# Optimization experiments

Hardware: AMD Instinct MI355X
Metric: run time of the kernel (lower is better)

Reference implementation:

```python
import jax, jax.numpy as jnp
import numpy as np

EPS_LN = 1e-5  # eqx.nn.LayerNorm default eps
DT_EPS = 1e-4  # softplus(dt) + 0.0001 in the module

H = 256  # hidden size
S = 256  # state size
B = 32
T = 4096


def setup_inputs() -> dict:
    key = jax.random.key(0)
    ks = jax.random.split(key, 8)
    sc = 1.0 / np.sqrt(H)
    return {
        "x": jax.random.normal(ks[0], (B, T, H), jnp.float32),
        "state0": jnp.zeros((B, S), jnp.float32),
        "in_to_state": jax.random.normal(ks[1], (S, H), jnp.float32) * sc,
        "state_to_hidden": jax.random.normal(ks[2], (H, S), jnp.float32) * sc,
        "direct": jax.random.normal(ks[3], (H,), jnp.float32) * sc,
        "a_diag": jax.random.normal(ks[4], (S,), jnp.float32),
        "g_diag": jax.random.normal(ks[5], (S,), jnp.float32),
        "dt": jax.random.normal(ks[6], (S,), jnp.float32) * 0.5 - 2.0,  # small timesteps
        "norm_w": jnp.ones((H,), jnp.float32),
        "norm_b": jnp.zeros((H,), jnp.float32),
        "out_w": jax.random.normal(ks[7], (H, H), jnp.float32) * sc,
        "out_b": jnp.zeros((H,), jnp.float32),
    }


def reference(x, state0, in_to_state, state_to_hidden, direct, a_diag, g_diag,
              dt, norm_w, norm_b, out_w, out_b):
    # Discretized diagonal oscillator coefficients (input-independent)
    dt_s = jax.nn.softplus(dt) + DT_EPS            # [S]
    omega = a_diag * dt_s                          # [S]
    decay = jnp.exp(-jax.nn.softplus(g_diag) * dt_s)
    decay = decay * decay                          # damped=True
    coeff = decay * jnp.cos(omega)                 # [S]

    # LayerNorm over feature dim (per-timestep, matching eqx.nn.LayerNorm)
    mu = jnp.mean(x, axis=-1, keepdims=True)
    var = jnp.var(x, axis=-1, keepdims=True)
    x_norm = (x - mu) * jax.lax.rsqrt(var + EPS_LN) * norm_w + norm_b  # [B,T,H]

    # Input injection: in_to_state @ x_norm for every timestep
    u = jnp.einsum("sh,bth->bts", in_to_state, x_norm)  # [B,T,S]

    # Diagonal linear recurrence: s_t = coeff * s_{t-1} + u_t
    def step(s, u_t):
        s = coeff * s + u_t
        return s, s

    u_t_major = jnp.swapaxes(u, 0, 1)                    # [T,B,S]
    final_state, states = jax.lax.scan(step, state0, u_t_major)
    states = jnp.swapaxes(states, 0, 1)                  # [B,T,S]

    # Readout + skip + gelu + out projection + residual
    mixed = jnp.einsum("hs,bts->bth", state_to_hidden, states) + direct * x_norm
    mixed = jax.nn.gelu(mixed)
    y = x + jnp.einsum("oh,bth->bto", out_w, mixed) + out_b
    return y, final_state
```

## Files before the change

### kernel.cpp

```cpp
#include <hip/hip_runtime.h>
#include <hip/hip_bf16.h>
#include <cstdint>
#include <cstddef>


typedef __bf16 bf16x8 __attribute__((ext_vector_type(8)));
typedef __bf16 bf16x4 __attribute__((ext_vector_type(4)));
typedef float  f32x4  __attribute__((ext_vector_type(4)));
typedef unsigned int u32x4 __attribute__((ext_vector_type(4)));

#define BB 32
#define TT 4096
#define HH 256
#define SS 256
#define MTOT (BB*TT)
#define NCHUNK 64
#define NT 8

__global__ void prep_kernel(const float* __restrict__ w1, const float* __restrict__ w2,
                            const float* __restrict__ w3,
                            __bf16* __restrict__ w1b, __bf16* __restrict__ w2b,
                            __bf16* __restrict__ w3b,
                            const float* __restrict__ a_diag, const float* __restrict__ g_diag,
                            const float* __restrict__ dt,
                            float* __restrict__ coeff, float* __restrict__ cL) {
    int i = blockIdx.x * 256 + threadIdx.x;
    w1b[i] = (__bf16)w1[i];
    w2b[i] = (__bf16)w2[i];
    w3b[i] = (__bf16)w3[i];
    if (i < SS) {
        float d = dt[i];
        float sp = (d > 20.f) ? d : log1pf(expf(d));
        float dts = sp + 1e-4f;
        float omega = a_diag[i] * dts;
        float gg = g_diag[i];
        float spg = (gg > 20.f) ? gg : log1pf(expf(gg));
        float dec = expf(-spg * dts);
        float c = dec * dec * cosf(omega);
        coeff[i] = c;
        float p = c;
        #pragma unroll
        for (int q = 0; q < 6; ++q) p = p * p;
        cL[i] = p;
    }
}

__device__ __forceinline__ void scan_xs_tile(__bf16* Xs, int tid, float c, float& st) {
    const int gb = tid >> 3, bo = (tid & 7) << 1;
    #pragma unroll
    for (int g4 = 0; g4 < 4; ++g4) {
        float v[8];
        #pragma unroll
        for (int r = 0; r < 8; ++r) {
            const int m = g4 * 8 + r;
            v[r] = (float)*(const __bf16*)((const char*)Xs + m * 512 + (((gb ^ (m & 15)) << 4) | bo));
        }
        __bf16 w[8];
        #pragma unroll
        for (int r = 0; r < 8; ++r) { st = c * st + v[r]; w[r] = (__bf16)st; }
        #pragma unroll
        for (int r = 0; r < 8; ++r) {
            const int m = g4 * 8 + r;
            *(__bf16*)((char*)Xs + m * 512 + (((gb ^ (m & 15)) << 4) | bo)) = w[r];
        }
    }
}

__device__ __forceinline__ void scan_es_carry(const __bf16* Es, int tid, float c, float& st) {
    const int gb = tid >> 2, bo = (tid & 3) << 1;
    #pragma unroll
    for (int g4 = 0; g4 < 4; ++g4) {
        float v[8];
        #pragma unroll
        for (int r = 0; r < 8; ++r) {
            const int m = g4 * 8 + r;
            v[r] = (float)*(const __bf16*)((const char*)Es + m * 512 + (((gb ^ ((m & 15) << 2)) << 3) | bo));
        }
        #pragma unroll
        for (int r = 0; r < 8; ++r) st = c * st + v[r];
    }
}

__global__ __launch_bounds__(512, 1) void gemm_ln_kernel(
    const __bf16* __restrict__ W,
    const float* __restrict__ x,
    const float* __restrict__ nw, const float* __restrict__ nb,
    __bf16* __restrict__ xn, __bf16* __restrict__ u,
    const float* __restrict__ coeff, const float* __restrict__ state0,
    float* __restrict__ carry)
{
    __shared__ __bf16 Xs[32 * 256];
    __shared__ __bf16 Es[32 * 256];

    const int tid  = threadIdx.x;
    const int lane = tid & 63;
    const int wid  = tid >> 6;
    const int l15  = lane & 15, quad = lane >> 4;

    bf16x8 Wf[2][8];
    #pragma unroll
    for (int jn = 0; jn < 2; ++jn) {
        const int n = wid * 32 + jn * 16 + l15;
        #pragma unroll
        for (int kb = 0; kb < 8; ++kb)
            Wf[jn][kb] = *(const bf16x8*)&W[(size_t)n * 256 + kb * 32 + quad * 8];
    }

    const int bxi = blockIdx.x;
    const int bb  = bxi >> 4;
    const int chb = (bxi & 15) * 4;
    float c_s = 0.f, s0v = 0.f;
    if (tid < 256) {
        c_s = coeff[tid];
        if (chb == 0) s0v = state0[(size_t)bb * 256 + tid];
    }

    const f32x4 wn4 = *(const f32x4*)&nw[lane * 4];
    const f32x4 bn4 = *(const f32x4*)&nb[lane * 4];

    const size_t mbase = (size_t)bxi * 256;

    f32x4 pf[4];
    auto ln_load = [&](int tile) {
        #pragma unroll
        for (int j = 0; j < 4; ++j) {
            const int m = j * 8 + wid;
            pf[j] = *(const f32x4*)&x[(mbase + (size_t)tile * 32 + m) * 256 + lane * 4];
        }
    };
    auto ln_store = [&](int tile) {
        #pragma unroll
        for (int j = 0; j < 4; ++j) {
            const int m = j * 8 + wid;
            f32x4 v = pf[j];
            float s  = v[0] + v[1] + v[2] + v[3];
            float ss = v[0]*v[0] + v[1]*v[1] + v[2]*v[2] + v[3]*v[3];
            #pragma unroll
            for (int off = 32; off; off >>= 1) {
                s  += __shfl_xor(s,  off, 64);
                ss += __shfl_xor(ss, off, 64);
            }
            float mu  = s * (1.f/256.f);
            float var = ss * (1.f/256.f) - mu * mu;
            float sc  = rsqrtf(var + 1e-5f);
            bf16x4 pk;
            #pragma unroll
            for (int q2 = 0; q2 < 4; ++q2)
                pk[q2] = (__bf16)((v[q2] - mu) * sc * wn4[q2] + bn4[q2]);
            *(bf16x4*)((char*)Xs + m * 512 + ((((lane >> 1) ^ (m & 15)) << 4) | ((lane & 1) << 3))) = pk;
            *(bf16x4*)&xn[(mbase + (size_t)tile * 32 + m) * 256 + lane * 4] = pk;
        }
    };

    ln_load(0);
    ln_store(0);
    __syncthreads();
    ln_load(1);

    const int hrow = tid >> 5;
    const int nc   = tid & 31;
    float stc = 0.f;

    for (int it = 0; it < NT; ++it) {
        const size_t mt0 = mbase + (size_t)it * 32;

        f32x4 acc[2][2] = {};
        #pragma unroll
        for (int kb = 0; kb < 8; ++kb) {
            bf16x8 xf[2];
            #pragma unroll
            for (int im = 0; im < 2; ++im)
                xf[im] = *(const bf16x8*)((const char*)Xs + (l15 + im * 16) * 512
                                          + (((kb * 4 + quad) ^ l15) * 16));
            #pragma unroll
            for (int jn = 0; jn < 2; ++jn)
                #pragma unroll
                for (int im = 0; im < 2; ++im)
                    acc[im][jn] = __builtin_amdgcn_mfma_f32_16x16x32_bf16(
                        Wf[jn][kb], xf[im], acc[im][jn], 0, 0, 0);
        }
        __syncthreads();

        if (it + 1 < NT) ln_store(it + 1);
        #pragma unroll
        for (int im = 0; im < 2; ++im) {
            const int m = l15 + im * 16;
            #pragma unroll
            for (int jn = 0; jn < 2; ++jn) {
                const int gn = wid * 8 + jn * 4 + quad;
                bf16x4 pk;
                #pragma unroll
                for (int r = 0; r < 4; ++r) pk[r] = (__bf16)acc[im][jn][r];
                *(bf16x4*)((char*)Es + m * 512 + ((gn ^ (l15 << 2)) * 8)) = pk;
            }
        }
        __syncthreads();

        if (it + 2 < NT) ln_load(it + 2);

        #pragma unroll
        for (int r = 0; r < 2; ++r) {
            const int m = r * 16 + hrow;
            bf16x8 ev = *(const bf16x8*)((const char*)Es + m * 512 + (((nc * 2) ^ (hrow << 2)) * 8));
            *(bf16x8*)&u[(mt0 + m) * 256 + nc * 8] = ev;
        }

        if (tid < 256) {
            if ((it & 1) == 0) stc = (it == 0 && chb == 0) ? s0v : 0.f;
            scan_es_carry(Es, tid, c_s, stc);
            if ((it & 1) == 1)
                carry[((size_t)bb * 64 + (chb + (it >> 1))) * 256 + tid] = stc;
        }
    }
}

__global__ __launch_bounds__(512, 1) void gemm_fused_kernel(
    const __bf16* __restrict__ W2, const __bf16* __restrict__ W3,
    const __bf16* __restrict__ u, const __bf16* __restrict__ xn,
    const float* __restrict__ dvec,
    const float* __restrict__ xres, const float* __restrict__ bias,
    const float* __restrict__ coeff, const float* __restrict__ state0,
    const float* __restrict__ carry,
    float* __restrict__ y)
{
    __shared__ __bf16 Xs [32 * 256];
    __shared__ __bf16 Es [32 * 256];
    __shared__ __bf16 Xs2[32 * 256];

    const int tid  = threadIdx.x;
    const int lane = tid & 63;
    const int wid  = tid >> 6;
    const int l15  = lane & 15, quad = lane >> 4;

    bf16x8 W2f[2][8];
    #pragma unroll
    for (int jn = 0; jn < 2; ++jn) {
        const int n = wid * 32 + jn * 16 + l15;
        #pragma unroll
        for (int kb = 0; kb < 8; ++kb)
            W2f[jn][kb] = *(const bf16x8*)&W2[(size_t)n * 256 + kb * 32 + quad * 8];
    }
    const __bf16* w3p0 = W3 + (size_t)(wid * 32 + l15) * 256 + quad * 8;
    const __bf16* w3p1 = w3p0 + 16 * 256;

    const int bxi = blockIdx.x;
    const int bb  = bxi >> 4;
    const int chb = (bxi & 15) * 4;
    float c_s = 0.f, cin0 = 0.f, cin1 = 0.f, cin2 = 0.f, cin3 = 0.f;
    if (tid < 256) {
        c_s  = coeff[tid];
        cin0 = (chb == 0) ? state0[(size_t)bb * 256 + tid]
                          : carry[((size_t)bb * 64 + chb - 1) * 256 + tid];
        cin1 = carry[((size_t)bb * 64 + chb + 0) * 256 + tid];
        cin2 = carry[((size_t)bb * 64 + chb + 1) * 256 + tid];
        cin3 = carry[((size_t)bb * 64 + chb + 2) * 256 + tid];
    }

    int sdst[2], srow[2];
    const int g = tid & 31;
    #pragma unroll
    for (int j = 0; j < 2; ++j) {
        const int m = j * 16 + (tid >> 5);
        srow[j] = m;
        sdst[j] = m * 512 + ((g ^ (m & 15)) * 16);
    }
    const int colb = g * 16;
    const size_t mbase = (size_t)bxi * 256;
    const char* Ub = (const char*)u;

    u32x4 pf[2];
    #pragma unroll
    for (int j = 0; j < 2; ++j)
        pf[j] = *(const u32x4*)(Ub + (mbase + srow[j]) * 512 + colb);
    #pragma unroll
    for (int j = 0; j < 2; ++j)
        *(u32x4*)((char*)Xs + sdst[j]) = pf[j];
    __syncthreads();
    #pragma unroll
    for (int j = 0; j < 2; ++j)
        pf[j] = *(const u32x4*)(Ub + (mbase + 32 + srow[j]) * 512 + colb);

    float st = 0.f;
    if (tid < 256) { st = cin0; scan_xs_tile(Xs, tid, c_s, st); }
    __syncthreads();

    const int hrow = tid >> 5;
    const int nc   = tid & 31;

    for (int it = 0; it < NT; ++it) {
        const size_t mt0 = mbase + (size_t)it * 32;

        f32x4 acc[2][2] = {};
        #pragma unroll
        for (int kb = 0; kb < 8; ++kb) {
            bf16x8 xf[2];
            #pragma unroll
            for (int im = 0; im < 2; ++im)
                xf[im] = *(const bf16x8*)((const char*)Xs + (l15 + im * 16) * 512
                                          + (((kb * 4 + quad) ^ l15) * 16));
            #pragma unroll
            for (int jn = 0; jn < 2; ++jn)
                #pragma unroll
                for (int im = 0; im < 2; ++im)
                    acc[im][jn] = __builtin_amdgcn_mfma_f32_16x16x32_bf16(
                        W2f[jn][kb], xf[im], acc[im][jn], 0, 0, 0);
        }
        __syncthreads();

        if (it + 1 < NT) {
            #pragma unroll
            for (int j = 0; j < 2; ++j)
                *(u32x4*)((char*)Xs + sdst[j]) = pf[j];
        }
        #pragma unroll
        for (int im = 0; im < 2; ++im) {
            const int m = l15 + im * 16;
            #pragma unroll
            for (int jn = 0; jn < 2; ++jn) {
                const int gn = wid * 8 + jn * 4 + quad;
                bf16x4 pk;
                #pragma unroll
                for (int r = 0; r < 4; ++r) pk[r] = (__bf16)acc[im][jn][r];
                *(bf16x4*)((char*)Es + m * 512 + ((gn ^ (l15 << 2)) * 8)) = pk;
            }
        }
        __syncthreads();

        if (it + 2 < NT) {
            #pragma unroll
            for (int j = 0; j < 2; ++j)
                pf[j] = *(const u32x4*)(Ub + (mt0 + 64 + srow[j]) * 512 + colb);
        }
        if (it + 1 < NT && tid < 256) {
            const int itt = it + 1;
            if ((itt & 1) == 0) {
                const int k = itt >> 1;
                st = (k == 1) ? cin1 : (k == 2) ? cin2 : cin3;
            }
            scan_xs_tile(Xs, tid, c_s, st);
        }

        #pragma unroll
        for (int r = 0; r < 2; ++r) {
            const int m = r * 16 + hrow;
            bf16x8 ev = *(const bf16x8*)((const char*)Es + m * 512 + (((nc * 2) ^ (hrow << 2)) * 8));
            const size_t gidx = (mt0 + m) * 256 + nc * 8;
            bf16x8 xv = *(const bf16x8*)&xn[gidx];
            f32x4 d0 = *(const f32x4*)&dvec[nc * 8];
            f32x4 d1 = *(const f32x4*)&dvec[nc * 8 + 4];
            bf16x8 pk;
            #pragma unroll
            for (int jj = 0; jj < 8; ++jj) {
                float dj = (jj < 4) ? d0[jj] : d1[jj - 4];
                float t = (float)ev[jj] + dj * (float)xv[jj];
                float q = t + 0.044715f * t * t * t;
                float e = __expf(-1.5957691216057308f * q);
                pk[jj] = (__bf16)(t * __builtin_amdgcn_rcpf(1.f + e));
            }
            *(bf16x8*)((char*)Xs2 + m * 512 + ((nc ^ (m & 15)) * 16)) = pk;
        }
        __syncthreads();

        f32x4 acc2[2][2] = {};
        bf16x8 wr[3][2];
        wr[0][0] = *(const bf16x8*)(w3p0);
        wr[0][1] = *(const bf16x8*)(w3p1);
        wr[1][0] = *(const bf16x8*)(w3p0 + 32);
        wr[1][1] = *(const bf16x8*)(w3p1 + 32);
        #pragma unroll
        for (int kb = 0; kb < 8; ++kb) {
            if (kb + 2 < 8) {
                wr[(kb + 2) % 3][0] = *(const bf16x8*)(w3p0 + (kb + 2) * 32);
                wr[(kb + 2) % 3][1] = *(const bf16x8*)(w3p1 + (kb + 2) * 32);
            }
            bf16x8 xf[2];
            #pragma unroll
            for (int im = 0; im < 2; ++im)
                xf[im] = *(const bf16x8*)((const char*)Xs2 + (l15 + im * 16) * 512
                                          + (((kb * 4 + quad) ^ l15) * 16));
            #pragma unroll
            for (int jn = 0; jn < 2; ++jn)
                #pragma unroll
                for (int im = 0; im < 2; ++im)
                    acc2[im][jn] = __builtin_amdgcn_mfma_f32_16x16x32_bf16(
                        wr[kb % 3][jn], xf[im], acc2[im][jn], 0, 0, 0);
        }
        __syncthreads();

        #pragma unroll
        for (int im = 0; im < 2; ++im) {
            const int m = l15 + im * 16;
            #pragma unroll
            for (int jn = 0; jn < 2; ++jn) {
                const int gn = wid * 8 + jn * 4 + quad;
                bf16x4 pk;
                #pragma unroll
                for (int r = 0; r < 4; ++r) pk[r] = (__bf16)acc2[im][jn][r];
                *(bf16x4*)((char*)Es + m * 512 + ((gn ^ (l15 << 2)) * 8)) = pk;
            }
        }
        __syncthreads();

        #pragma unroll
        for (int r = 0; r < 2; ++r) {
            const int m = r * 16 + hrow;
            bf16x8 ev = *(const bf16x8*)((const char*)Es + m * 512 + (((nc * 2) ^ (hrow << 2)) * 8));
            const size_t gidx = (mt0 + m) * 256 + nc * 8;
            f32x4 x0 = *(const f32x4*)&xres[gidx];
            f32x4 x1 = *(const f32x4*)&xres[gidx + 4];
            f32x4 b0 = *(const f32x4*)&bias[nc * 8];
            f32x4 b1 = *(const f32x4*)&bias[nc * 8 + 4];
            f32x4 y0, y1;
            #pragma unroll
            for (int jj = 0; jj < 4; ++jj) {
                y0[jj] = x0[jj] + (float)ev[jj]     + b0[jj];
                y1[jj] = x1[jj] + (float)ev[jj + 4] + b1[jj];
            }
            *(f32x4*)&y[gidx]     = y0;
            *(f32x4*)&y[gidx + 4] = y1;
        }
    }
}

__global__ __launch_bounds__(256) void scan_prefix(float* carry, const float* __restrict__ cL,
                            float* __restrict__ fs_out) {
    int b = blockIdx.x, s = threadIdx.x;
    float cl = cL[s];
    float P = 0.f;
    #pragma unroll
    for (int jo = 0; jo < 8; ++jo) {
        float v[8];
        #pragma unroll
        for (int r = 0; r < 8; ++r)
            v[r] = carry[((size_t)b * NCHUNK + jo * 8 + r) * SS + s];
        float w[8];
        #pragma unroll
        for (int r = 0; r < 8; ++r) { P = cl * P + v[r]; w[r] = P; }
        #pragma unroll
        for (int r = 0; r < 8; ++r)
            carry[((size_t)b * NCHUNK + jo * 8 + r) * SS + s] = w[r];
    }
    fs_out[b * SS + s] = P;
}

extern "C" void kernel_launch(void* const* d_in, const int* in_sizes, int n_in,
                              void* d_out, int out_size, void* d_ws, size_t ws_size,
                              hipStream_t stream) {
    const float* x      = (const float*)d_in[0];
    const float* state0 = (const float*)d_in[1];
    const float* w1     = (const float*)d_in[2];
    const float* w2     = (const float*)d_in[3];
    const float* direct = (const float*)d_in[4];
    const float* a_diag = (const float*)d_in[5];
    const float* g_diag = (const float*)d_in[6];
    const float* dt     = (const float*)d_in[7];
    const float* norm_w = (const float*)d_in[8];
    const float* norm_b = (const float*)d_in[9];
    const float* w3     = (const float*)d_in[10];
    const float* out_b  = (const float*)d_in[11];

    char* ws = (char*)d_ws;
    const size_t MH2 = (size_t)MTOT * HH * 2;
    __bf16* xn    = (__bf16*)(ws);
    __bf16* u     = (__bf16*)(ws + MH2);
    __bf16* w1b   = (__bf16*)(ws + 2*MH2);
    __bf16* w2b   = (__bf16*)(ws + 2*MH2 + 131072);
    __bf16* w3b   = (__bf16*)(ws + 2*MH2 + 262144);
    float*  coeff = (float*)(ws + 2*MH2 + 393216);
    float*  cL    = (float*)(ws + 2*MH2 + 394240);
    float*  carry = (float*)(ws + 2*MH2 + 395264);

    float* y_out  = (float*)d_out;
    float* fs_out = (float*)d_out + (size_t)MTOT * HH;

    prep_kernel<<<256, 256, 0, stream>>>(w1, w2, w3, w1b, w2b, w3b,
                                         a_diag, g_diag, dt, coeff, cL);
    gemm_ln_kernel<<<512, 512, 0, stream>>>(w1b, x, norm_w, norm_b, xn, u,
                                            coeff, state0, carry);
    scan_prefix<<<BB, 256, 0, stream>>>(carry, cL, fs_out);
    gemm_fused_kernel<<<512, 512, 0, stream>>>(w2b, w3b, u, xn, direct, x, out_b,
                                               coeff, state0, carry, y_out);
}
```

Baseline: 373.0 us.

## Recompute LayerNorm in fused kernel instead of storing xn, use 64-row tiles

Stops writing the bf16 normalized activations to global memory in the first kernel. The fused kernel instead recomputes LayerNorm from the fp32 input it already loads for the residual, with a 32-lane shuffle reduction per row. This removes a full-size write and read of xn at the cost of extra ALU and shuffle work. The M-tile also grows from 32 to 64 rows, with 4 iterations each covering one scan chunk, which doubles the LDS buffers and the accumulator registers.

```diff
diff --git a/kernel.cpp b/kernel.cpp
--- a/kernel.cpp
+++ b/kernel.cpp
@@ -15,7 +15,7 @@
 #define SS 256
 #define MTOT (BB*TT)
 #define NCHUNK 64
-#define NT 8
+#define NT 4
 
 __global__ void prep_kernel(const float* __restrict__ w1, const float* __restrict__ w2,
                             const float* __restrict__ w3,
@@ -45,14 +45,14 @@
     }
 }
 
-__device__ __forceinline__ void scan_xs_tile(__bf16* Xs, int tid, float c, float& st) {
+__device__ __forceinline__ void scan_xs_tile64(__bf16* Xs, int tid, float c, float& st) {
     const int gb = tid >> 3, bo = (tid & 7) << 1;
     #pragma unroll
-    for (int g4 = 0; g4 < 4; ++g4) {
+    for (int g8 = 0; g8 < 8; ++g8) {
         float v[8];
         #pragma unroll
         for (int r = 0; r < 8; ++r) {
-            const int m = g4 * 8 + r;
+            const int m = g8 * 8 + r;
             v[r] = (float)*(const __bf16*)((const char*)Xs + m * 512 + (((gb ^ (m & 15)) << 4) | bo));
         }
         __bf16 w[8];
@@ -60,20 +60,20 @@
         for (int r = 0; r < 8; ++r) { st = c * st + v[r]; w[r] = (__bf16)st; }
         #pragma unroll
         for (int r = 0; r < 8; ++r) {
-            const int m = g4 * 8 + r;
+            const int m = g8 * 8 + r;
             *(__bf16*)((char*)Xs + m * 512 + (((gb ^ (m & 15)) << 4) | bo)) = w[r];
         }
     }
 }
 
-__device__ __forceinline__ void scan_es_carry(const __bf16* Es, int tid, float c, float& st) {
+__device__ __forceinline__ void scan_es_carry64(const __bf16* Es, int tid, float c, float& st) {
     const int gb = tid >> 2, bo = (tid & 3) << 1;
     #pragma unroll
-    for (int g4 = 0; g4 < 4; ++g4) {
+    for (int g8 = 0; g8 < 8; ++g8) {
         float v[8];
         #pragma unroll
         for (int r = 0; r < 8; ++r) {
-            const int m = g4 * 8 + r;
+            const int m = g8 * 8 + r;
             v[r] = (float)*(const __bf16*)((const char*)Es + m * 512 + (((gb ^ ((m & 15) << 2)) << 3) | bo));
         }
         #pragma unroll
@@ -85,12 +85,12 @@
     const __bf16* __restrict__ W,
     const float* __restrict__ x,
     const float* __restrict__ nw, const float* __restrict__ nb,
-    __bf16* __restrict__ xn, __bf16* __restrict__ u,
+    __bf16* __restrict__ u,
     const float* __restrict__ coeff, const float* __restrict__ state0,
     float* __restrict__ carry)
 {
-    __shared__ __bf16 Xs[32 * 256];
-    __shared__ __bf16 Es[32 * 256];
+    __shared__ __bf16 Xs[64 * 256];
+    __shared__ __bf16 Es[64 * 256];
 
     const int tid  = threadIdx.x;
     const int lane = tid & 63;
@@ -120,17 +120,17 @@
 
     const size_t mbase = (size_t)bxi * 256;
 
-    f32x4 pf[4];
+    f32x4 pf[8];
     auto ln_load = [&](int tile) {
         #pragma unroll
-        for (int j = 0; j < 4; ++j) {
+        for (int j = 0; j < 8; ++j) {
             const int m = j * 8 + wid;
-            pf[j] = *(const f32x4*)&x[(mbase + (size_t)tile * 32 + m) * 256 + lane * 4];
+            pf[j] = *(const f32x4*)&x[(mbase + (size_t)tile * 64 + m) * 256 + lane * 4];
         }
     };
-    auto ln_store = [&](int tile) {
-        #pragma unroll
-        for (int j = 0; j < 4; ++j) {
+    auto ln_store = [&]() {
+        #pragma unroll
+        for (int j = 0; j < 8; ++j) {
             const int m = j * 8 + wid;
             f32x4 v = pf[j];
             float s  = v[0] + v[1] + v[2] + v[3];
@@ -148,42 +148,40 @@
             for (int q2 = 0; q2 < 4; ++q2)
                 pk[q2] = (__bf16)((v[q2] - mu) * sc * wn4[q2] + bn4[q2]);
             *(bf16x4*)((char*)Xs + m * 512 + ((((lane >> 1) ^ (m & 15)) << 4) | ((lane & 1) << 3))) = pk;
-            *(bf16x4*)&xn[(mbase + (size_t)tile * 32 + m) * 256 + lane * 4] = pk;
         }
     };
 
     ln_load(0);
-    ln_store(0);
+    ln_store();
     __syncthreads();
     ln_load(1);
 
     const int hrow = tid >> 5;
     const int nc   = tid & 31;
-    float stc = 0.f;
 
     for (int it = 0; it < NT; ++it) {
-        const size_t mt0 = mbase + (size_t)it * 32;
-
-        f32x4 acc[2][2] = {};
+        const size_t mt0 = mbase + (size_t)it * 64;
+
+        f32x4 acc[4][2] = {};
         #pragma unroll
         for (int kb = 0; kb < 8; ++kb) {
-            bf16x8 xf[2];
-            #pragma unroll
-            for (int im = 0; im < 2; ++im)
+            bf16x8 xf[4];
+            #pragma unroll
+            for (int im = 0; im < 4; ++im)
                 xf[im] = *(const bf16x8*)((const char*)Xs + (l15 + im * 16) * 512
                                           + (((kb * 4 + quad) ^ l15) * 16));
             #pragma unroll
             for (int jn = 0; jn < 2; ++jn)
                 #pragma unroll
-                for (int im = 0; im < 2; ++im)
+                for (int im = 0; im < 4; ++im)
                     acc[im][jn] = __builtin_amdgcn_mfma_f32_16x16x32_bf16(
                         Wf[jn][kb], xf[im], acc[im][jn], 0, 0, 0);
         }
         __syncthreads();
 
-        if (it + 1 < NT) ln_store(it + 1);
-        #pragma unroll
-        for (int im = 0; im < 2; ++im) {
+        if (it + 1 < NT) ln_store();
+        #pragma unroll
+        for (int im = 0; im < 4; ++im) {
             const int m = l15 + im * 16;
             #pragma unroll
             for (int jn = 0; jn < 2; ++jn) {
@@ -199,33 +197,33 @@
         if (it + 2 < NT) ln_load(it + 2);
 
         #pragma unroll
-        for (int r = 0; r < 2; ++r) {
+        for (int r = 0; r < 4; ++r) {
             const int m = r * 16 + hrow;
             bf16x8 ev = *(const bf16x8*)((const char*)Es + m * 512 + (((nc * 2) ^ (hrow << 2)) * 8));
             *(bf16x8*)&u[(mt0 + m) * 256 + nc * 8] = ev;
         }
 
         if (tid < 256) {
-            if ((it & 1) == 0) stc = (it == 0 && chb == 0) ? s0v : 0.f;
-            scan_es_carry(Es, tid, c_s, stc);
-            if ((it & 1) == 1)
-                carry[((size_t)bb * 64 + (chb + (it >> 1))) * 256 + tid] = stc;
+            float stc = (it == 0 && chb == 0) ? s0v : 0.f;
+            scan_es_carry64(Es, tid, c_s, stc);
+            carry[((size_t)bb * 64 + (chb + it)) * 256 + tid] = stc;
         }
     }
 }
 
 __global__ __launch_bounds__(512, 1) void gemm_fused_kernel(
     const __bf16* __restrict__ W2, const __bf16* __restrict__ W3,
-    const __bf16* __restrict__ u, const __bf16* __restrict__ xn,
+    const __bf16* __restrict__ u,
+    const float* __restrict__ nw, const float* __restrict__ nb,
     const float* __restrict__ dvec,
     const float* __restrict__ xres, const float* __restrict__ bias,
     const float* __restrict__ coeff, const float* __restrict__ state0,
     const float* __restrict__ carry,
     float* __restrict__ y)
 {
-    __shared__ __bf16 Xs [32 * 256];
-    __shared__ __bf16 Es [32 * 256];
-    __shared__ __bf16 Xs2[32 * 256];
+    __shared__ __bf16 Xs [64 * 256];
+    __shared__ __bf16 Es [64 * 256];
+    __shared__ __bf16 Xs2[64 * 256];
 
     const int tid  = threadIdx.x;
     const int lane = tid & 63;
@@ -256,52 +254,61 @@
         cin3 = carry[((size_t)bb * 64 + chb + 2) * 256 + tid];
     }
 
-    int sdst[2], srow[2];
-    const int g = tid & 31;
-    #pragma unroll
-    for (int j = 0; j < 2; ++j) {
-        const int m = j * 16 + (tid >> 5);
-        srow[j] = m;
-        sdst[j] = m * 512 + ((g ^ (m & 15)) * 16);
-    }
-    const int colb = g * 16;
+    const int hrow = tid >> 5;
+    const int nc   = tid & 31;
+
+    const f32x4 wn0 = *(const f32x4*)&nw[nc * 8];
+    const f32x4 wn1 = *(const f32x4*)&nw[nc * 8 + 4];
+    const f32x4 bn0 = *(const f32x4*)&nb[nc * 8];
+    const f32x4 bn1 = *(const f32x4*)&nb[nc * 8 + 4];
+    const f32x4 d0  = *(const f32x4*)&dvec[nc * 8];
+    const f32x4 d1  = *(const f32x4*)&dvec[nc * 8 + 4];
+    const f32x4 b0  = *(const f32x4*)&bias[nc * 8];
+    const f32x4 b1  = *(const f32x4*)&bias[nc * 8 + 4];
+
+    int sdst[4], srow[4], scolb[4];
+    #pragma unroll
+    for (int j = 0; j < 4; ++j) {
+        int o = wid * 256 + j * 64 + lane;
+        int m = o >> 5, g = o & 31;
+        srow[j]  = m;
+        scolb[j] = g * 16;
+        sdst[j]  = m * 512 + ((g ^ (m & 15)) * 16);
+    }
     const size_t mbase = (size_t)bxi * 256;
     const char* Ub = (const char*)u;
 
-    u32x4 pf[2];
-    #pragma unroll
-    for (int j = 0; j < 2; ++j)
-        pf[j] = *(const u32x4*)(Ub + (mbase + srow[j]) * 512 + colb);
-    #pragma unroll
-    for (int j = 0; j < 2; ++j)
+    u32x4 pf[4];
+    #pragma unroll
+    for (int j = 0; j < 4; ++j)
+        pf[j] = *(const u32x4*)(Ub + (mbase + srow[j]) * 512 + scolb[j]);
+    #pragma unroll
+    for (int j = 0; j < 4; ++j)
         *(u32x4*)((char*)Xs + sdst[j]) = pf[j];
     __syncthreads();
     #pragma unroll
-    for (int j = 0; j < 2; ++j)
-        pf[j] = *(const u32x4*)(Ub + (mbase + 32 + srow[j]) * 512 + colb);
+    for (int j = 0; j < 4; ++j)
+        pf[j] = *(const u32x4*)(Ub + (mbase + 64 + srow[j]) * 512 + scolb[j]);
 
     float st = 0.f;
-    if (tid < 256) { st = cin0; scan_xs_tile(Xs, tid, c_s, st); }
+    if (tid < 256) { st = cin0; scan_xs_tile64(Xs, tid, c_s, st); }
     __syncthreads();
 
-    const int hrow = tid >> 5;
-    const int nc   = tid & 31;
-
     for (int it = 0; it < NT; ++it) {
-        const size_t mt0 = mbase + (size_t)it * 32;
-
-        f32x4 acc[2][2] = {};
+        const size_t mt0 = mbase + (size_t)it * 64;
+
+        f32x4 acc[4][2] = {};
         #pragma unroll
         for (int kb = 0; kb < 8; ++kb) {
-            bf16x8 xf[2];
-            #pragma unroll
-            for (int im = 0; im < 2; ++im)
+            bf16x8 xf[4];
+            #pragma unroll
+            for (int im = 0; im < 4; ++im)
                 xf[im] = *(const bf16x8*)((const char*)Xs + (l15 + im * 16) * 512
                                           + (((kb * 4 + quad) ^ l15) * 16));
             #pragma unroll
             for (int jn = 0; jn < 2; ++jn)
                 #pragma unroll
-                for (int im = 0; im < 2; ++im)
+                for (int im = 0; im < 4; ++im)
                     acc[im][jn] = __builtin_amdgcn_mfma_f32_16x16x32_bf16(
                         W2f[jn][kb], xf[im], acc[im][jn], 0, 0, 0);
         }
@@ -309,11 +316,11 @@
 
         if (it + 1 < NT) {
             #pragma unroll
-            for (int j = 0; j < 2; ++j)
+            for (int j = 0; j < 4; ++j)
                 *(u32x4*)((char*)Xs + sdst[j]) = pf[j];
         }
         #pragma unroll
-        for (int im = 0; im < 2; ++im) {
+        for (int im = 0; im < 4; ++im) {
             const int m = l15 + im * 16;
             #pragma unroll
             for (int jn = 0; jn < 2; ++jn) {
@@ -328,31 +335,41 @@
 
         if (it + 2 < NT) {
             #pragma unroll
-            for (int j = 0; j < 2; ++j)
-                pf[j] = *(const u32x4*)(Ub + (mt0 + 64 + srow[j]) * 512 + colb);
+            for (int j = 0; j < 4; ++j)
+                pf[j] = *(const u32x4*)(Ub + (mt0 + 128 + srow[j]) * 512 + scolb[j]);
         }
         if (it + 1 < NT && tid < 256) {
-            const int itt = it + 1;
-            if ((itt & 1) == 0) {
-                const int k = itt >> 1;
-                st = (k == 1) ? cin1 : (k == 2) ? cin2 : cin3;
-            }
-            scan_xs_tile(Xs, tid, c_s, st);
-        }
-
-        #pragma unroll
-        for (int r = 0; r < 2; ++r) {
+            st = (it == 0) ? cin1 : (it == 1) ? cin2 : cin3;
+            scan_xs_tile64(Xs, tid, c_s, st);
+        }
+
+        #pragma unroll
+        for (int r = 0; r < 4; ++r) {
             const int m = r * 16 + hrow;
             bf16x8 ev = *(const bf16x8*)((const char*)Es + m * 512 + (((nc * 2) ^ (hrow << 2)) * 8));
             const size_t gidx = (mt0 + m) * 256 + nc * 8;
-            bf16x8 xv = *(const bf16x8*)&xn[gidx];
-            f32x4 d0 = *(const f32x4*)&dvec[nc * 8];
-            f32x4 d1 = *(const f32x4*)&dvec[nc * 8 + 4];
+            f32x4 x0 = *(const f32x4*)&xres[gidx];
+            f32x4 x1 = *(const f32x4*)&xres[gidx + 4];
+            float s  = x0[0]+x0[1]+x0[2]+x0[3] + x1[0]+x1[1]+x1[2]+x1[3];
+            float ss = x0[0]*x0[0]+x0[1]*x0[1]+x0[2]*x0[2]+x0[3]*x0[3]
+                     + x1[0]*x1[0]+x1[1]*x1[1]+x1[2]*x1[2]+x1[3]*x1[3];
+            #pragma unroll
+            for (int off = 16; off; off >>= 1) {
+                s  += __shfl_xor(s,  off, 64);
+                ss += __shfl_xor(ss, off, 64);
+            }
+            float mu  = s * (1.f/256.f);
+            float var = ss * (1.f/256.f) - mu * mu;
+            float rs  = rsqrtf(var + 1e-5f);
             bf16x8 pk;
             #pragma unroll
             for (int jj = 0; jj < 8; ++jj) {
-                float dj = (jj < 4) ? d0[jj] : d1[jj - 4];
-                float t = (float)ev[jj] + dj * (float)xv[jj];
+                float xj = (jj < 4) ? x0[jj] : x1[jj - 4];
+                float wj = (jj < 4) ? wn0[jj] : wn1[jj - 4];
+                float bj = (jj < 4) ? bn0[jj] : bn1[jj - 4];
+                float dj = (jj < 4) ? d0[jj]  : d1[jj - 4];
+                float xnj = (xj - mu) * rs * wj + bj;
+                float t = (float)ev[jj] + dj * xnj;
                 float q = t + 0.044715f * t * t * t;
                 float e = __expf(-1.5957691216057308f * q);
                 pk[jj] = (__bf16)(t * __builtin_amdgcn_rcpf(1.f + e));
@@ -361,7 +378,7 @@
         }
         __syncthreads();
 
-        f32x4 acc2[2][2] = {};
+        f32x4 acc2[4][2] = {};
         bf16x8 wr[3][2];
         wr[0][0] = *(const bf16x8*)(w3p0);
         wr[0][1] = *(const bf16x8*)(w3p1);
@@ -373,22 +390,22 @@
                 wr[(kb + 2) % 3][0] = *(const bf16x8*)(w3p0 + (kb + 2) * 32);
                 wr[(kb + 2) % 3][1] = *(const bf16x8*)(w3p1 + (kb + 2) * 32);
             }
-            bf16x8 xf[2];
-            #pragma unroll
-            for (int im = 0; im < 2; ++im)
+            bf16x8 xf[4];
+            #pragma unroll
+            for (int im = 0; im < 4; ++im)
                 xf[im] = *(const bf16x8*)((const char*)Xs2 + (l15 + im * 16) * 512
                                           + (((kb * 4 + quad) ^ l15) * 16));
             #pragma unroll
             for (int jn = 0; jn < 2; ++jn)
                 #pragma unroll
-                for (int im = 0; im < 2; ++im)
+                for (int im = 0; im < 4; ++im)
                     acc2[im][jn] = __builtin_amdgcn_mfma_f32_16x16x32_bf16(
                         wr[kb % 3][jn], xf[im], acc2[im][jn], 0, 0, 0);
         }
         __syncthreads();
 
         #pragma unroll
-        for (int im = 0; im < 2; ++im) {
+        for (int im = 0; im < 4; ++im) {
             const int m = l15 + im * 16;
             #pragma unroll
             for (int jn = 0; jn < 2; ++jn) {
@@ -402,14 +419,12 @@
         __syncthreads();
 
         #pragma unroll
-        for (int r = 0; r < 2; ++r) {
+        for (int r = 0; r < 4; ++r) {
             const int m = r * 16 + hrow;
             bf16x8 ev = *(const bf16x8*)((const char*)Es + m * 512 + (((nc * 2) ^ (hrow << 2)) * 8));
             const size_t gidx = (mt0 + m) * 256 + nc * 8;
             f32x4 x0 = *(const f32x4*)&xres[gidx];
             f32x4 x1 = *(const f32x4*)&xres[gidx + 4];
-            f32x4 b0 = *(const f32x4*)&bias[nc * 8];
-            f32x4 b1 = *(const f32x4*)&bias[nc * 8 + 4];
             f32x4 y0, y1;
             #pragma unroll
             for (int jj = 0; jj < 4; ++jj) {
@@ -461,23 +476,22 @@
 
     char* ws = (char*)d_ws;
     const size_t MH2 = (size_t)MTOT * HH * 2;
-    __bf16* xn    = (__bf16*)(ws);
-    __bf16* u     = (__bf16*)(ws + MH2);
-    __bf16* w1b   = (__bf16*)(ws + 2*MH2);
-    __bf16* w2b   = (__bf16*)(ws + 2*MH2 + 131072);
-    __bf16* w3b   = (__bf16*)(ws + 2*MH2 + 262144);
-    float*  coeff = (float*)(ws + 2*MH2 + 393216);
-    float*  cL    = (float*)(ws + 2*MH2 + 394240);
-    float*  carry = (float*)(ws + 2*MH2 + 395264);
+    __bf16* u     = (__bf16*)(ws);
+    __bf16* w1b   = (__bf16*)(ws + MH2);
+    __bf16* w2b   = (__bf16*)(ws + MH2 + 131072);
+    __bf16* w3b   = (__bf16*)(ws + MH2 + 262144);
+    float*  coeff = (float*)(ws + MH2 + 393216);
+    float*  cL    = (float*)(ws + MH2 + 394240);
+    float*  carry = (float*)(ws + MH2 + 395264);
 
     float* y_out  = (float*)d_out;
     float* fs_out = (float*)d_out + (size_t)MTOT * HH;
 
     prep_kernel<<<256, 256, 0, stream>>>(w1, w2, w3, w1b, w2b, w3b,
                                          a_diag, g_diag, dt, coeff, cL);
-    gemm_ln_kernel<<<512, 512, 0, stream>>>(w1b, x, norm_w, norm_b, xn, u,
+    gemm_ln_kernel<<<512, 512, 0, stream>>>(w1b, x, norm_w, norm_b, u,
                                             coeff, state0, carry);
     scan_prefix<<<BB, 256, 0, stream>>>(carry, cL, fs_out);
-    gemm_fused_kernel<<<512, 512, 0, stream>>>(w2b, w3b, u, xn, direct, x, out_b,
-                                               coeff, state0, carry, y_out);
-}
+    gemm_fused_kernel<<<512, 512, 0, stream>>>(w2b, w3b, u, norm_w, norm_b, direct,
+                                               x, out_b, coeff, state0, carry, y_out);
+}
```

After: 409.7 us. +9.9%, slower.

## Recompute LayerNorm in fused kernel instead of storing normalized activations

Applied to the files above, without the earlier changes.

The first kernel no longer writes the bf16 normalized activations to global memory. The fused second kernel rereads x in fp32 and recomputes the LayerNorm statistics with a 32-lane shuffle reduction before the skip and GELU step. This drops a 64MB write and a 64MB read but adds a 128MB fp32 read of x (later reused for the residual) plus some extra ALU work. It also loads all eight W3 fragments up front instead of using a three-deep rotating prefetch, which raises register use.

```diff
diff --git a/kernel.cpp b/kernel.cpp
--- a/kernel.cpp
+++ b/kernel.cpp
@@ -85,7 +85,7 @@
     const __bf16* __restrict__ W,
     const float* __restrict__ x,
     const float* __restrict__ nw, const float* __restrict__ nb,
-    __bf16* __restrict__ xn, __bf16* __restrict__ u,
+    __bf16* __restrict__ u,
     const float* __restrict__ coeff, const float* __restrict__ state0,
     float* __restrict__ carry)
 {
@@ -128,7 +128,7 @@
             pf[j] = *(const f32x4*)&x[(mbase + (size_t)tile * 32 + m) * 256 + lane * 4];
         }
     };
-    auto ln_store = [&](int tile) {
+    auto ln_store = [&]() {
         #pragma unroll
         for (int j = 0; j < 4; ++j) {
             const int m = j * 8 + wid;
@@ -148,12 +148,11 @@
             for (int q2 = 0; q2 < 4; ++q2)
                 pk[q2] = (__bf16)((v[q2] - mu) * sc * wn4[q2] + bn4[q2]);
             *(bf16x4*)((char*)Xs + m * 512 + ((((lane >> 1) ^ (m & 15)) << 4) | ((lane & 1) << 3))) = pk;
-            *(bf16x4*)&xn[(mbase + (size_t)tile * 32 + m) * 256 + lane * 4] = pk;
         }
     };
 
     ln_load(0);
-    ln_store(0);
+    ln_store();
     __syncthreads();
     ln_load(1);
 
@@ -181,7 +180,7 @@
         }
         __syncthreads();
 
-        if (it + 1 < NT) ln_store(it + 1);
+        if (it + 1 < NT) ln_store();
         #pragma unroll
         for (int im = 0; im < 2; ++im) {
             const int m = l15 + im * 16;
@@ -216,7 +215,8 @@
 
 __global__ __launch_bounds__(512, 1) void gemm_fused_kernel(
     const __bf16* __restrict__ W2, const __bf16* __restrict__ W3,
-    const __bf16* __restrict__ u, const __bf16* __restrict__ xn,
+    const __bf16* __restrict__ u,
+    const float* __restrict__ nw, const float* __restrict__ nb,
     const float* __restrict__ dvec,
     const float* __restrict__ xres, const float* __restrict__ bias,
     const float* __restrict__ coeff, const float* __restrict__ state0,
@@ -345,14 +345,34 @@
             const int m = r * 16 + hrow;
             bf16x8 ev = *(const bf16x8*)((const char*)Es + m * 512 + (((nc * 2) ^ (hrow << 2)) * 8));
             const size_t gidx = (mt0 + m) * 256 + nc * 8;
-            bf16x8 xv = *(const bf16x8*)&xn[gidx];
-            f32x4 d0 = *(const f32x4*)&dvec[nc * 8];
-            f32x4 d1 = *(const f32x4*)&dvec[nc * 8 + 4];
+            f32x4 x0 = *(const f32x4*)&xres[gidx];
+            f32x4 x1 = *(const f32x4*)&xres[gidx + 4];
+            float s  = x0[0]+x0[1]+x0[2]+x0[3] + x1[0]+x1[1]+x1[2]+x1[3];
+            float ss = x0[0]*x0[0]+x0[1]*x0[1]+x0[2]*x0[2]+x0[3]*x0[3]
+                     + x1[0]*x1[0]+x1[1]*x1[1]+x1[2]*x1[2]+x1[3]*x1[3];
+            #pragma unroll
+            for (int off = 16; off; off >>= 1) {
+                s  += __shfl_xor(s,  off, 64);
+                ss += __shfl_xor(ss, off, 64);
+            }
+            float mu  = s * (1.f/256.f);
+            float var = ss * (1.f/256.f) - mu * mu;
+            float rs  = rsqrtf(var + 1e-5f);
+            const f32x4 wn0 = *(const f32x4*)&nw[nc * 8];
+            const f32x4 wn1 = *(const f32x4*)&nw[nc * 8 + 4];
+            const f32x4 bn0 = *(const f32x4*)&nb[nc * 8];
+            const f32x4 bn1 = *(const f32x4*)&nb[nc * 8 + 4];
+            const f32x4 d0  = *(const f32x4*)&dvec[nc * 8];
+            const f32x4 d1  = *(const f32x4*)&dvec[nc * 8 + 4];
             bf16x8 pk;
             #pragma unroll
             for (int jj = 0; jj < 8; ++jj) {
-                float dj = (jj < 4) ? d0[jj] : d1[jj - 4];
-                float t = (float)ev[jj] + dj * (float)xv[jj];
+                float xj = (jj < 4) ? x0[jj] : x1[jj - 4];
+                float wj = (jj < 4) ? wn0[jj] : wn1[jj - 4];
+                float bj = (jj < 4) ? bn0[jj] : bn1[jj - 4];
+                float dj = (jj < 4) ? d0[jj]  : d1[jj - 4];
+                float xnj = (xj - mu) * rs * wj + bj;
+                float t = (float)ev[jj] + dj * xnj;
                 float q = t + 0.044715f * t * t * t;
                 float e = __expf(-1.5957691216057308f * q);
                 pk[jj] = (__bf16)(t * __builtin_amdgcn_rcpf(1.f + e));
@@ -362,17 +382,14 @@
         __syncthreads();
 
         f32x4 acc2[2][2] = {};
-        bf16x8 wr[3][2];
-        wr[0][0] = *(const bf16x8*)(w3p0);
-        wr[0][1] = *(const bf16x8*)(w3p1);
-        wr[1][0] = *(const bf16x8*)(w3p0 + 32);
-        wr[1][1] = *(const bf16x8*)(w3p1 + 32);
+        bf16x8 wr[8][2];
         #pragma unroll
         for (int kb = 0; kb < 8; ++kb) {
-            if (kb + 2 < 8) {
-                wr[(kb + 2) % 3][0] = *(const bf16x8*)(w3p0 + (kb + 2) * 32);
-                wr[(kb + 2) % 3][1] = *(const bf16x8*)(w3p1 + (kb + 2) * 32);
-            }
+            wr[kb][0] = *(const bf16x8*)(w3p0 + kb * 32);
+            wr[kb][1] = *(const bf16x8*)(w3p1 + kb * 32);
+        }
+        #pragma unroll
+        for (int kb = 0; kb < 8; ++kb) {
             bf16x8 xf[2];
             #pragma unroll
             for (int im = 0; im < 2; ++im)
@@ -383,7 +400,7 @@
                 #pragma unroll
                 for (int im = 0; im < 2; ++im)
                     acc2[im][jn] = __builtin_amdgcn_mfma_f32_16x16x32_bf16(
-                        wr[kb % 3][jn], xf[im], acc2[im][jn], 0, 0, 0);
+                        wr[kb][jn], xf[im], acc2[im][jn], 0, 0, 0);
         }
         __syncthreads();
 
@@ -408,8 +425,8 @@
             const size_t gidx = (mt0 + m) * 256 + nc * 8;
             f32x4 x0 = *(const f32x4*)&xres[gidx];
             f32x4 x1 = *(const f32x4*)&xres[gidx + 4];
-            f32x4 b0 = *(const f32x4*)&bias[nc * 8];
-            f32x4 b1 = *(const f32x4*)&bias[nc * 8 + 4];
+            const f32x4 b0 = *(const f32x4*)&bias[nc * 8];
+            const f32x4 b1 = *(const f32x4*)&bias[nc * 8 + 4];
             f32x4 y0, y1;
             #pragma unroll
             for (int jj = 0; jj < 4; ++jj) {
@@ -461,23 +478,22 @@
 
     char* ws = (char*)d_ws;
     const size_t MH2 = (size_t)MTOT * HH * 2;
-    __bf16* xn    = (__bf16*)(ws);
-    __bf16* u     = (__bf16*)(ws + MH2);
-    __bf16* w1b   = (__bf16*)(ws + 2*MH2);
-    __bf16* w2b   = (__bf16*)(ws + 2*MH2 + 131072);
-    __bf16* w3b   = (__bf16*)(ws + 2*MH2 + 262144);
-    float*  coeff = (float*)(ws + 2*MH2 + 393216);
-    float*  cL    = (float*)(ws + 2*MH2 + 394240);
-    float*  carry = (float*)(ws + 2*MH2 + 395264);
+    __bf16* u     = (__bf16*)(ws);
+    __bf16* w1b   = (__bf16*)(ws + MH2);
+    __bf16* w2b   = (__bf16*)(ws + MH2 + 131072);
+    __bf16* w3b   = (__bf16*)(ws + MH2 + 262144);
+    float*  coeff = (float*)(ws + MH2 + 393216);
+    float*  cL    = (float*)(ws + MH2 + 394240);
+    float*  carry = (float*)(ws + MH2 + 395264);
 
     float* y_out  = (float*)d_out;
     float* fs_out = (float*)d_out + (size_t)MTOT * HH;
 
     prep_kernel<<<256, 256, 0, stream>>>(w1, w2, w3, w1b, w2b, w3b,
                                          a_diag, g_diag, dt, coeff, cL);
-    gemm_ln_kernel<<<512, 512, 0, stream>>>(w1b, x, norm_w, norm_b, xn, u,
+    gemm_ln_kernel<<<512, 512, 0, stream>>>(w1b, x, norm_w, norm_b, u,
                                             coeff, state0, carry);
     scan_prefix<<<BB, 256, 0, stream>>>(carry, cL, fs_out);
-    gemm_fused_kernel<<<512, 512, 0, stream>>>(w2b, w3b, u, xn, direct, x, out_b,
-                                               coeff, state0, carry, y_out);
-}
+    gemm_fused_kernel<<<512, 512, 0, stream>>>(w2b, w3b, u, norm_w, norm_b, direct,
+                                               x, out_b, coeff, state0, carry, y_out);
+}
```

New measurement: 409.7 us. 1.1x slower.
